# Kernel tuning notes

Hardware: AMD Instinct MI355X
Metric: run time of the kernel (lower is better)

## Reference

```python
import jax, jax.numpy as jnp
import numpy as np

D_MODEL = 1024
NUM_HEADS = 16
D_K = D_MODEL // NUM_HEADS
TEMPERATURE = 1.0
LN_EPS = 1e-5


def setup_inputs() -> dict:
    key = jax.random.key(0)
    ks = jax.random.split(key, 12)
    B, S, D = 4, 1024, D_MODEL
    w = lambda k: jax.random.normal(k, (D, D), dtype=jnp.float32) * 0.02
    b = lambda k: jax.random.normal(k, (D,), dtype=jnp.float32) * 0.01
    return {
        "query": jax.random.normal(ks[0], (B, S, D), dtype=jnp.float32),
        "key": jax.random.normal(ks[1], (B, S, D), dtype=jnp.float32),
        "value": jax.random.normal(ks[2], (B, S, D), dtype=jnp.float32),
        "wq": w(ks[3]), "bq": b(ks[4]),
        "wk": w(ks[5]), "bk": b(ks[6]),
        "wv": w(ks[7]), "bv": b(ks[8]),
        "wo": w(ks[9]), "bo": b(ks[10]),
        "temporal_bias": jax.random.normal(ks[11], (1, 1, NUM_HEADS, 1, 1), dtype=jnp.float32) * 0.01,
        "adaptive_temp": jnp.ones((1,), dtype=jnp.float32),
        "ln_gamma": jnp.ones((D,), dtype=jnp.float32),
        "ln_beta": jnp.zeros((D,), dtype=jnp.float32),
    }


def reference(query, key, value, wq, bq, wk, bk, wv, bv, wo, bo,
              temporal_bias, adaptive_temp, ln_gamma, ln_beta):
    B, S, D = query.shape
    H, dk = NUM_HEADS, D_K
    # QKV projections -> (B, H, S, dk)
    Q = (query @ wq.T + bq).reshape(B, S, H, dk).transpose(0, 2, 1, 3)
    K = (key @ wk.T + bk).reshape(B, S, H, dk).transpose(0, 2, 1, 3)
    V = (value @ wv.T + bv).reshape(B, S, H, dk).transpose(0, 2, 1, 3)
    scores = jnp.einsum('bhqd,bhkd->bhqk', Q, K) / jnp.sqrt(jnp.float32(dk))
    scores = scores / (TEMPERATURE * adaptive_temp)
    # torch broadcasting bug reproduced: (B,H,S,S) + (1,1,H,1,1) -> (1,B,H,S,S)
    scores5 = scores[None, ...] + temporal_bias  # (1, B, H, S, S)
    attn = jax.nn.softmax(scores5, axis=-1)      # (1, B, H, S, S)
    ctx5 = jnp.einsum('xbhqk,bhkd->xbhqd', attn, V)  # (1, B, H, S, dk)
    # torch: transpose(1,2) -> (1, H, B, S, dk), then view(B, S, D)
    ctx = jnp.swapaxes(ctx5, 1, 2).reshape(B, S, D)
    out = ctx @ wo.T + bo
    y = out + query
    mu = jnp.mean(y, axis=-1, keepdims=True)
    var = jnp.mean(jnp.square(y - mu), axis=-1, keepdims=True)
    out_ln = (y - mu) / jnp.sqrt(var + LN_EPS) * ln_gamma + ln_beta
    return out_ln, attn
```

## Files before the change

kernel.cpp:

```cpp
#include <hip/hip_runtime.h>
#include <math.h>

#define BB 4
#define SS 1024
#define DD 1024
#define HH 16
#define DKK 64
#define NN (BB*SS)
#define LN_EPS 1e-5f
#define QB 128
#define JB 64

typedef __attribute__((ext_vector_type(8))) short bf16x8;
typedef __attribute__((ext_vector_type(4))) float f32x4;
typedef __attribute__((address_space(3))) unsigned int lds_u32;
typedef const __attribute__((address_space(1))) unsigned int glb_u32;

static __device__ __forceinline__ unsigned short f2bf(float x){
    unsigned int u = __float_as_uint(x);
    u += 0x7fff + ((u >> 16) & 1);
    return (unsigned short)(u >> 16);
}
static __device__ __forceinline__ int swzp(int q){
    return ((q & 7) << 4) ^ ((q & 8) << 2);
}
static __device__ __forceinline__ void sync_lds_only(){
    __builtin_amdgcn_sched_barrier(0);
    asm volatile("s_waitcnt lgkmcnt(0)" ::: "memory");
    __builtin_amdgcn_s_barrier();
    __builtin_amdgcn_sched_barrier(0);
}

__global__ __launch_bounds__(256)
void k_cvt_all(const float* __restrict__ q, const float* __restrict__ k,
               const float* __restrict__ v, const float* __restrict__ w0,
               const float* __restrict__ w1, const float* __restrict__ w2,
               const float* __restrict__ w3, unsigned short* __restrict__ xout,
               unsigned short* __restrict__ wout){
    const int bidx = blockIdx.x;
    const float* src; unsigned short* dst; size_t i;
    if (bidx < 6144) {
        const int z = bidx >> 11, bi = bidx & 2047;
        src = (z == 0) ? q : (z == 1) ? k : v;
        dst = xout + (size_t)z*NN*DD;
        i = ((size_t)bi*256 + threadIdx.x)*8;
    } else {
        const int z = (bidx - 6144) >> 9, bi = (bidx - 6144) & 511;
        src = (z == 0) ? w0 : (z == 1) ? w1 : (z == 2) ? w2 : w3;
        dst = wout + (size_t)z*DD*DD;
        i = ((size_t)bi*256 + threadIdx.x)*8;
    }
    float4 a = *reinterpret_cast<const float4*>(&src[i]);
    float4 b = *reinterpret_cast<const float4*>(&src[i+4]);
    int4 w;
    w.x = (int)((unsigned)f2bf(a.x) | ((unsigned)f2bf(a.y) << 16));
    w.y = (int)((unsigned)f2bf(a.z) | ((unsigned)f2bf(a.w) << 16));
    w.z = (int)((unsigned)f2bf(b.x) | ((unsigned)f2bf(b.y) << 16));
    w.w = (int)((unsigned)f2bf(b.z) | ((unsigned)f2bf(b.w) << 16));
    *reinterpret_cast<int4*>(&dst[i]) = w;
}

__global__ __launch_bounds__(256)
void k_gemmqkv(const unsigned short* __restrict__ Xb, const unsigned short* __restrict__ Wb,
               const float* __restrict__ b0, const float* __restrict__ b1,
               const float* __restrict__ b2, unsigned short* __restrict__ outb)
{
    __shared__ __align__(16) unsigned short Als[128*32];
    __shared__ __align__(16) unsigned short Bls[128*32];
    __shared__ __align__(16) unsigned short Cs[128*128];
    const int z = blockIdx.z;
    const unsigned short* X = Xb + (size_t)z*NN*DD;
    const unsigned short* W = Wb + (size_t)z*DD*DD;
    const float* bias = (z == 0) ? b0 : (z == 1) ? b1 : b2;
    unsigned short* out = outb + (size_t)z*NN*DD;

    const int row0 = blockIdx.x * 128;
    const int col0 = blockIdx.y * 128;
    const int t = threadIdx.x;
    const int w = t >> 6, l = t & 63;
    const int wr = w >> 1, wc = w & 1;

    f32x4 acc[4][4];
    #pragma unroll
    for (int m=0;m<4;++m)
        #pragma unroll
        for (int n=0;n<4;++n) acc[m][n] = (f32x4){0.f,0.f,0.f,0.f};

    const int srow  = l >> 2;
    const int skoff = (l & 3) * 8;

    for (int kt = 0; kt < DD; kt += 32) {
        #pragma unroll
        for (int i=0;i<2;++i) {
            const unsigned short* ga = X + (size_t)(row0 + w*32 + i*16 + srow)*DD + kt + skoff;
            const unsigned short* gb = W + (size_t)(col0 + w*32 + i*16 + srow)*DD + kt + skoff;
            __builtin_amdgcn_global_load_lds((glb_u32*)ga, (lds_u32*)&Als[(w*2+i)*512], 16, 0, 0);
            __builtin_amdgcn_global_load_lds((glb_u32*)gb, (lds_u32*)&Bls[(w*2+i)*512], 16, 0, 0);
        }
        __syncthreads();
        bf16x8 af[4], bfr[4];
        #pragma unroll
        for (int m=0;m<4;++m)
            af[m] = *reinterpret_cast<const bf16x8*>(&Als[(wr*64 + m*16 + (l&15))*32 + (l>>4)*8]);
        #pragma unroll
        for (int n=0;n<4;++n)
            bfr[n] = *reinterpret_cast<const bf16x8*>(&Bls[(wc*64 + n*16 + (l&15))*32 + (l>>4)*8]);
        __builtin_amdgcn_s_setprio(1);
        #pragma unroll
        for (int m=0;m<4;++m)
            #pragma unroll
            for (int n=0;n<4;++n)
                acc[m][n] = __builtin_amdgcn_mfma_f32_16x16x32_bf16(af[m], bfr[n], acc[m][n], 0, 0, 0);
        __builtin_amdgcn_s_setprio(0);
        __syncthreads();
    }

    if (z < 2) {
        #pragma unroll
        for (int m=0;m<4;++m){
            const int trb = wr*64 + m*16 + ((l>>4)<<2);
            #pragma unroll
            for (int n=0;n<4;++n){
                const int tc = wc*64 + n*16 + (l&15);
                const float bc = bias[col0 + tc];
                #pragma unroll
                for (int r=0;r<4;++r){
                    const int tr = trb + r;
                    *reinterpret_cast<unsigned short*>(
                        (char*)Cs + ((tr*256 + tc*2) ^ ((tr & 12) << 3))) = f2bf(acc[m][n][r] + bc);
                }
            }
        }
        __syncthreads();
        #pragma unroll
        for (int i=0;i<8;++i){
            const int slot = i*256 + t;
            const int r2 = slot >> 4, g = slot & 15;
            int4 v = *reinterpret_cast<const int4*>(
                (char*)Cs + ((r2*256 + g*16) ^ ((r2 & 12) << 3)));
            *reinterpret_cast<int4*>(&out[(size_t)(row0 + r2)*DD + col0 + g*8]) = v;
        }
    } else {
        #pragma unroll
        for (int m=0;m<4;++m){
            const int trb = wr*64 + m*16 + ((l>>4)<<2);
            #pragma unroll
            for (int n=0;n<4;++n){
                const int tc = wc*64 + n*16 + (l&15);
                const float bc = bias[col0 + tc];
                ushort4 pk;
                pk.x = f2bf(acc[m][n][0] + bc);
                pk.y = f2bf(acc[m][n][1] + bc);
                pk.z = f2bf(acc[m][n][2] + bc);
                pk.w = f2bf(acc[m][n][3] + bc);
                *reinterpret_cast<ushort4*>(
                    (char*)Cs + ((tc*256 + trb*2) ^ ((tc & 15) << 3))) = pk;
            }
        }
        __syncthreads();
        const int b = row0 >> 10;
        const int sbase = row0 & 1023;
        #pragma unroll
        for (int i=0;i<16;++i){
            const int cr = i*8 + (t>>5);
            const int ch = t & 31;
            ushort4 v = *reinterpret_cast<const ushort4*>(
                (char*)Cs + ((cr*256 + ch*8) ^ ((cr & 15) << 3)));
            const int gc = col0 + cr, h = gc >> 6, k = gc & 63;
            *reinterpret_cast<ushort4*>(
                &out[(((size_t)b*HH + h)*DKK + k)*SS + sbase + ch*4]) = v;
        }
    }
}

__global__ __launch_bounds__(512)
void k_attn(const unsigned short* __restrict__ Qb, const unsigned short* __restrict__ Kb,
            const unsigned short* __restrict__ Vtb, const float* __restrict__ at,
            float* __restrict__ attn, unsigned short* __restrict__ ctxb)
{
    __shared__ __align__(16) unsigned short Qs[QB*64];
    __shared__ __align__(16) unsigned short Ks[2][JB*64];
    __shared__ __align__(16) unsigned short Vs[2][DKK*JB];
    __shared__ __align__(16) unsigned short Ps[QB*JB];
    const int f   = blockIdx.x;
    const int wk2 = (f & 7)*64 + (f >> 3);
    const int bh  = wk2 >> 3;
    const int q0  = (wk2 & 7) * QB;
    const int b = bh >> 4, h = bh & 15;
    const int t = threadIdx.x, w = t >> 6, l = t & 63;
    const float alpha = 0.125f / at[0];

    const unsigned short* Qg = Qb  + (size_t)b*SS*DD + (size_t)h*64;
    const unsigned short* Kg = Kb  + (size_t)b*SS*DD + (size_t)h*64;
    const unsigned short* Vg = Vtb + (size_t)bh*DKK*SS;

    const int sj  = t >> 3;
    const int skc = (t & 7) * 8;

    #pragma unroll
    for (int p = 0; p < 2; ++p) {
        const int c = t + p*512;
        const int q = c >> 3, kc = (c & 7) * 8;
        int4 v = *reinterpret_cast<const int4*>(&Qg[(size_t)(q0 + q)*DD + kc]);
        *reinterpret_cast<int4*>((char*)Qs + ((q*128 + kc*2) ^ ((q & 7) << 4))) = v;
    }
    {
        int4 kv = *reinterpret_cast<const int4*>(&Kg[(size_t)sj*DD + skc]);
        *reinterpret_cast<int4*>((char*)Ks[0] + ((sj*128 + skc*2) ^ ((sj & 7) << 4))) = kv;
    }
    __syncthreads();
    bf16x8 qf[2];
    {
        const int q = w*16 + (l & 15);
        #pragma unroll
        for (int ks = 0; ks < 2; ++ks)
            qf[ks] = *reinterpret_cast<const bf16x8*>(
                (char*)Qs + ((q*128 + (l>>4)*16 + ks*64) ^ ((q & 7) << 4)));
    }

    float srow = 0.f;
    int cur = 0;
    for (int j0 = 0; j0 < SS; j0 += JB) {
        int4 knext;
        const bool more = (j0 + JB < SS);
        if (more)
            knext = *reinterpret_cast<const int4*>(&Kg[(size_t)(j0 + JB + sj)*DD + skc]);
        f32x4 acc[4];
        #pragma unroll
        for (int n = 0; n < 4; ++n) acc[n] = (f32x4){0.f,0.f,0.f,0.f};
        __builtin_amdgcn_s_setprio(1);
        #pragma unroll
        for (int ks = 0; ks < 2; ++ks) {
            #pragma unroll
            for (int n = 0; n < 4; ++n) {
                const int j = n*16 + (l & 15);
                bf16x8 kf = *reinterpret_cast<const bf16x8*>(
                    (char*)Ks[cur] + ((j*128 + (l>>4)*16 + ks*64) ^ ((j & 7) << 4)));
                acc[n] = __builtin_amdgcn_mfma_f32_16x16x32_bf16(kf, qf[ks], acc[n], 0, 0, 0);
            }
        }
        __builtin_amdgcn_s_setprio(0);
        float ps = 0.f;
        #pragma unroll
        for (int n = 0; n < 4; ++n)
            #pragma unroll
            for (int r = 0; r < 4; ++r) ps += __expf(acc[n][r]*alpha);
        srow += ps;
        if (more)
            *reinterpret_cast<int4*>((char*)Ks[cur^1] + ((sj*128 + skc*2) ^ ((sj & 7) << 4))) = knext;
        __syncthreads();
        cur ^= 1;
    }
    srow += __shfl_xor(srow, 16, 64);
    srow += __shfl_xor(srow, 32, 64);
    const float sinv = 1.0f / srow;

    f32x4 cacc[4];
    #pragma unroll
    for (int n = 0; n < 4; ++n) cacc[n] = (f32x4){0.f,0.f,0.f,0.f};

    int4 knext, vnext;
    {
        int4 kv = *reinterpret_cast<const int4*>(&Kg[(size_t)sj*DD + skc]);
        int4 vv = *reinterpret_cast<const int4*>(&Vg[(size_t)sj*SS + skc]);
        *reinterpret_cast<int4*>((char*)Ks[0] + ((sj*128 + skc*2) ^ ((sj & 7) << 4))) = kv;
        *reinterpret_cast<int4*>((char*)Vs[0] + ((sj*128 + skc*2) ^ ((sj & 7) << 4))) = vv;
        knext = *reinterpret_cast<const int4*>(&Kg[(size_t)(JB + sj)*DD + skc]);
        vnext = *reinterpret_cast<const int4*>(&Vg[(size_t)sj*SS + JB + skc]);
    }
    __syncthreads();

    cur = 0;
    for (int j0 = 0; j0 < SS; j0 += JB) {
        const bool more = (j0 + JB < SS);
        f32x4 acc[4];
        #pragma unroll
        for (int n = 0; n < 4; ++n) acc[n] = (f32x4){0.f,0.f,0.f,0.f};
        __builtin_amdgcn_s_setprio(1);
        #pragma unroll
        for (int ks = 0; ks < 2; ++ks) {
            #pragma unroll
            for (int n = 0; n < 4; ++n) {
                const int j = n*16 + (l & 15);
                bf16x8 kf = *reinterpret_cast<const bf16x8*>(
                    (char*)Ks[cur] + ((j*128 + (l>>4)*16 + ks*64) ^ ((j & 7) << 4)));
                acc[n] = __builtin_amdgcn_mfma_f32_16x16x32_bf16(kf, qf[ks], acc[n], 0, 0, 0);
            }
        }
        __builtin_amdgcn_s_setprio(0);
        {
            const int q = w*16 + (l & 15);
            const int c = l >> 4;
            #pragma unroll
            for (int n = 0; n < 4; ++n) {
                float p0 = __expf(acc[n][0]*alpha) * sinv;
                float p1 = __expf(acc[n][1]*alpha) * sinv;
                float p2 = __expf(acc[n][2]*alpha) * sinv;
                float p3 = __expf(acc[n][3]*alpha) * sinv;
                int2 pk;
                pk.x = (int)((unsigned)f2bf(p0) | ((unsigned)f2bf(p1) << 16));
                pk.y = (int)((unsigned)f2bf(p2) | ((unsigned)f2bf(p3) << 16));
                *reinterpret_cast<int2*>(
                    (char*)Ps + ((q*128 + n*32 + c*8) ^ swzp(q))) = pk;
            }
        }
        if (more) {
            *reinterpret_cast<int4*>((char*)Ks[cur^1] + ((sj*128 + skc*2) ^ ((sj & 7) << 4))) = knext;
            *reinterpret_cast<int4*>((char*)Vs[cur^1] + ((sj*128 + skc*2) ^ ((sj & 7) << 4))) = vnext;
        }
        sync_lds_only();
        if (j0 + 2*JB < SS) {
            knext = *reinterpret_cast<const int4*>(&Kg[(size_t)(j0 + 2*JB + sj)*DD + skc]);
            vnext = *reinterpret_cast<const int4*>(&Vg[(size_t)sj*SS + j0 + 2*JB + skc]);
        }
        __builtin_amdgcn_s_setprio(1);
        #pragma unroll
        for (int ks = 0; ks < 2; ++ks) {
            const int qr = w*16 + (l & 15);
            bf16x8 pf = *reinterpret_cast<const bf16x8*>(
                (char*)Ps + ((qr*128 + (l>>4)*16 + ks*64) ^ swzp(qr)));
            #pragma unroll
            for (int n = 0; n < 4; ++n) {
                const int d = n*16 + (l & 15);
                bf16x8 vf = *reinterpret_cast<const bf16x8*>(
                    (char*)Vs[cur] + ((d*128 + (l>>4)*16 + ks*64) ^ ((d & 7) << 4)));
                cacc[n] = __builtin_amdgcn_mfma_f32_16x16x32_bf16(pf, vf, cacc[n], 0, 0, 0);
            }
        }
        __builtin_amdgcn_s_setprio(0);
        #pragma unroll
        for (int i = 0; i < 4; ++i) {
            const int sr = i*32 + (t >> 4);
            const int j4 = (t & 15) * 4;
            int2 u = *reinterpret_cast<const int2*>(
                (char*)Ps + ((sr*128 + j4*2) ^ swzp(sr)));
            f32x4 fv;
            fv.x = __uint_as_float(((unsigned)u.x) << 16);
            fv.y = __uint_as_float(((unsigned)u.x) & 0xffff0000u);
            fv.z = __uint_as_float(((unsigned)u.y) << 16);
            fv.w = __uint_as_float(((unsigned)u.y) & 0xffff0000u);
            __builtin_nontemporal_store(fv, reinterpret_cast<f32x4*>(
                &attn[((size_t)bh*SS + q0 + sr)*SS + j0 + j4]));
        }
        sync_lds_only();
        cur ^= 1;
    }

    #pragma unroll
    for (int n = 0; n < 4; ++n) {
        const int d = n*16 + (l & 15);
        #pragma unroll
        for (int r = 0; r < 4; ++r) {
            const int q = q0 + w*16 + (l>>4)*4 + r;
            ctxb[(((size_t)h*BB + b)*SS + q)*DKK + d] = f2bf(cacc[n][r]);
        }
    }
}

__global__ __launch_bounds__(256)
void k_gemmo(const unsigned short* __restrict__ X, const unsigned short* __restrict__ W,
             const float* __restrict__ bias, const float* __restrict__ resid,
             float* __restrict__ outf)
{
    __shared__ __align__(16) unsigned short Als[128*32];
    __shared__ __align__(16) unsigned short Bls[128*32];
    const int row0 = blockIdx.x * 128;
    const int col0 = blockIdx.y * 128;
    const int t = threadIdx.x;
    const int w = t >> 6, l = t & 63;
    const int wr = w >> 1, wc = w & 1;

    f32x4 acc[4][4];
    #pragma unroll
    for (int m=0;m<4;++m)
        #pragma unroll
        for (int n=0;n<4;++n) acc[m][n] = (f32x4){0.f,0.f,0.f,0.f};

    const int srow  = l >> 2;
    const int skoff = (l & 3) * 8;

    for (int kt = 0; kt < DD; kt += 32) {
        #pragma unroll
        for (int i=0;i<2;++i) {
            const unsigned short* ga = X + (size_t)(row0 + w*32 + i*16 + srow)*DD + kt + skoff;
            const unsigned short* gb = W + (size_t)(col0 + w*32 + i*16 + srow)*DD + kt + skoff;
            __builtin_amdgcn_global_load_lds((glb_u32*)ga, (lds_u32*)&Als[(w*2+i)*512], 16, 0, 0);
            __builtin_amdgcn_global_load_lds((glb_u32*)gb, (lds_u32*)&Bls[(w*2+i)*512], 16, 0, 0);
        }
        __syncthreads();
        bf16x8 af[4], bfr[4];
        #pragma unroll
        for (int m=0;m<4;++m)
            af[m] = *reinterpret_cast<const bf16x8*>(&Als[(wr*64 + m*16 + (l&15))*32 + (l>>4)*8]);
        #pragma unroll
        for (int n=0;n<4;++n)
            bfr[n] = *reinterpret_cast<const bf16x8*>(&Bls[(wc*64 + n*16 + (l&15))*32 + (l>>4)*8]);
        __builtin_amdgcn_s_setprio(1);
        #pragma unroll
        for (int m=0;m<4;++m)
            #pragma unroll
            for (int n=0;n<4;++n)
                acc[m][n] = __builtin_amdgcn_mfma_f32_16x16x32_bf16(af[m], bfr[n], acc[m][n], 0, 0, 0);
        __builtin_amdgcn_s_setprio(0);
        __syncthreads();
    }

    #pragma unroll
    for (int m=0;m<4;++m){
        const int grow_base = row0 + wr*64 + m*16 + ((l>>4)<<2);
        #pragma unroll
        for (int n=0;n<4;++n){
            const int col = col0 + wc*64 + n*16 + (l&15);
            const float bc = bias[col];
            #pragma unroll
            for (int r=0;r<4;++r){
                const int row = grow_base + r;
                outf[(size_t)row*DD + col] = acc[m][n][r] + bc + resid[(size_t)row*DD + col];
            }
        }
    }
}

__global__ __launch_bounds__(256)
void k_ln(const float* __restrict__ y, const float* __restrict__ g,
          const float* __restrict__ be, float* __restrict__ out)
{
    const int row = blockIdx.x;
    const int t = threadIdx.x;
    float4 v = *reinterpret_cast<const float4*>(&y[(size_t)row*DD + t*4]);
    float s  = v.x + v.y + v.z + v.w;
    float ss = v.x*v.x + v.y*v.y + v.z*v.z + v.w*v.w;
    #pragma unroll
    for (int off = 32; off > 0; off >>= 1) {
        s  += __shfl_xor(s,  off, 64);
        ss += __shfl_xor(ss, off, 64);
    }
    __shared__ float red[8];
    const int lane = t & 63, wid = t >> 6;
    if (lane == 0) { red[wid] = s; red[4+wid] = ss; }
    __syncthreads();
    const float S1 = red[0]+red[1]+red[2]+red[3];
    const float S2 = red[4]+red[5]+red[6]+red[7];
    const float mu  = S1 * (1.0f/DD);
    const float var = fmaxf(S2 * (1.0f/DD) - mu*mu, 0.0f);
    const float rstd = rsqrtf(var + LN_EPS);
    float4 gv = *reinterpret_cast<const float4*>(&g[t*4]);
    float4 bv = *reinterpret_cast<const float4*>(&be[t*4]);
    float4 o;
    o.x = (v.x - mu)*rstd*gv.x + bv.x;
    o.y = (v.y - mu)*rstd*gv.y + bv.y;
    o.z = (v.z - mu)*rstd*gv.z + bv.z;
    o.w = (v.w - mu)*rstd*gv.w + bv.w;
    *reinterpret_cast<float4*>(&out[(size_t)row*DD + t*4]) = o;
}

extern "C" void kernel_launch(void* const* d_in, const int* in_sizes, int n_in,
                              void* d_out, int out_size, void* d_ws, size_t ws_size,
                              hipStream_t stream) {
    const float* query = (const float*)d_in[0];
    const float* key   = (const float*)d_in[1];
    const float* value = (const float*)d_in[2];
    const float* wq = (const float*)d_in[3];
    const float* bq = (const float*)d_in[4];
    const float* wk = (const float*)d_in[5];
    const float* bk = (const float*)d_in[6];
    const float* wv = (const float*)d_in[7];
    const float* bv = (const float*)d_in[8];
    const float* wo = (const float*)d_in[9];
    const float* bo = (const float*)d_in[10];
    const float* at = (const float*)d_in[12];
    const float* g  = (const float*)d_in[13];
    const float* be = (const float*)d_in[14];

    float* out_ln = (float*)d_out;
    float* attn   = (float*)d_out + (size_t)NN*DD;

    char* wsb = (char*)d_ws;
    unsigned short* xq   = (unsigned short*)(wsb);
    unsigned short* Qb   = (unsigned short*)(wsb + ((size_t)24<<20));
    unsigned short* Kb   = (unsigned short*)(wsb + ((size_t)32<<20));
    unsigned short* Vtb  = (unsigned short*)(wsb + ((size_t)40<<20));
    unsigned short* ctxb = (unsigned short*)(wsb + ((size_t)48<<20));
    unsigned short* wqb  = (unsigned short*)(wsb + ((size_t)56<<20));
    float*          y    = (float*)(wsb);

    k_cvt_all<<<8192, 256, 0, stream>>>(query, key, value, wq, wk, wv, wo, xq, wqb);

    k_gemmqkv<<<dim3(32, 8, 3), 256, 0, stream>>>(xq, wqb, bq, bk, bv, Qb);

    k_attn<<<dim3(512), 512, 0, stream>>>(Qb, Kb, Vtb, at, attn, ctxb);

    k_gemmo<<<dim3(32, 8), 256, 0, stream>>>(ctxb, wqb + (size_t)3*DD*DD, bo, query, y);

    k_ln<<<NN, 256, 0, stream>>>(y, g, be, out_ln);
}
```

Baseline: 175.0 us.

## Split softmax row-sum pass into separate high-parallelism kernel

Moves the first pass of the attention kernel (QK^T plus exp row sums) into a new k_sums kernel. It launches 2048 blocks, each covering 64 queries and half the key range, and writes partial sums to workspace. k_attn then loads Q fragments straight from global memory and reads the two partial sums, so only the second pass remains. The aim is more parallelism and occupancy for the reduction pass. In exchange it adds a kernel launch and a small workspace round trip, and recomputes QK^T just as the old first pass did.

```diff
diff --git a/kernel.cpp b/kernel.cpp
--- a/kernel.cpp
+++ b/kernel.cpp
@@ -173,12 +173,90 @@
     }
 }
 
+__global__ __launch_bounds__(256)
+void k_sums(const unsigned short* __restrict__ Qb, const unsigned short* __restrict__ Kb,
+            const float* __restrict__ at, float* __restrict__ rsums)
+{
+    __shared__ __align__(16) unsigned short Ks[2][JB*64];
+    const int f   = blockIdx.x;
+    const int swz = (f & 7)*256 + (f >> 3);
+    const int bh  = swz >> 5;
+    const int qt  = (swz >> 1) & 15;
+    const int jh  = swz & 1;
+    const int b = bh >> 4, h = bh & 15;
+    const int t = threadIdx.x, w = t >> 6, l = t & 63;
+    const float alpha = 0.125f / at[0];
+
+    const unsigned short* Qg = Qb + (size_t)b*SS*DD + (size_t)h*64;
+    const unsigned short* Kg = Kb + (size_t)b*SS*DD + (size_t)h*64;
+    const int q0 = qt*64;
+    const int jbase = jh*512;
+
+    const int sj  = t >> 2;
+    const int skc = (t & 3) * 16;
+
+    bf16x8 qf[2];
+    const int qrow = q0 + w*16 + (l & 15);
+    #pragma unroll
+    for (int ks = 0; ks < 2; ++ks)
+        qf[ks] = *reinterpret_cast<const bf16x8*>(
+            &Qg[(size_t)qrow*DD + ks*32 + (l>>4)*8]);
+
+    {
+        int4 kv0 = *reinterpret_cast<const int4*>(&Kg[(size_t)(jbase + sj)*DD + skc]);
+        int4 kv1 = *reinterpret_cast<const int4*>(&Kg[(size_t)(jbase + sj)*DD + skc + 8]);
+        *reinterpret_cast<int4*>((char*)Ks[0] + ((sj*128 + skc*2)      ^ ((sj & 7) << 4))) = kv0;
+        *reinterpret_cast<int4*>((char*)Ks[0] + ((sj*128 + skc*2 + 16) ^ ((sj & 7) << 4))) = kv1;
+    }
+    __syncthreads();
+
+    float srow = 0.f;
+    int cur = 0;
+    for (int jt = 0; jt < 512; jt += JB) {
+        int4 k0, k1;
+        const bool more = (jt + JB < 512);
+        if (more) {
+            k0 = *reinterpret_cast<const int4*>(&Kg[(size_t)(jbase + jt + JB + sj)*DD + skc]);
+            k1 = *reinterpret_cast<const int4*>(&Kg[(size_t)(jbase + jt + JB + sj)*DD + skc + 8]);
+        }
+        f32x4 acc[4];
+        #pragma unroll
+        for (int n = 0; n < 4; ++n) acc[n] = (f32x4){0.f,0.f,0.f,0.f};
+        __builtin_amdgcn_s_setprio(1);
+        #pragma unroll
+        for (int ks = 0; ks < 2; ++ks) {
+            #pragma unroll
+            for (int n = 0; n < 4; ++n) {
+                const int j = n*16 + (l & 15);
+                bf16x8 kf = *reinterpret_cast<const bf16x8*>(
+                    (char*)Ks[cur] + ((j*128 + (l>>4)*16 + ks*64) ^ ((j & 7) << 4)));
+                acc[n] = __builtin_amdgcn_mfma_f32_16x16x32_bf16(kf, qf[ks], acc[n], 0, 0, 0);
+            }
+        }
+        __builtin_amdgcn_s_setprio(0);
+        #pragma unroll
+        for (int n = 0; n < 4; ++n)
+            #pragma unroll
+            for (int r = 0; r < 4; ++r) srow += __expf(acc[n][r]*alpha);
+        if (more) {
+            *reinterpret_cast<int4*>((char*)Ks[cur^1] + ((sj*128 + skc*2)      ^ ((sj & 7) << 4))) = k0;
+            *reinterpret_cast<int4*>((char*)Ks[cur^1] + ((sj*128 + skc*2 + 16) ^ ((sj & 7) << 4))) = k1;
+        }
+        __syncthreads();
+        cur ^= 1;
+    }
+    srow += __shfl_xor(srow, 16, 64);
+    srow += __shfl_xor(srow, 32, 64);
+    if ((l >> 4) == 0)
+        rsums[((size_t)bh*2 + jh)*SS + qrow] = srow;
+}
+
 __global__ __launch_bounds__(512)
 void k_attn(const unsigned short* __restrict__ Qb, const unsigned short* __restrict__ Kb,
             const unsigned short* __restrict__ Vtb, const float* __restrict__ at,
+            const float* __restrict__ rsums,
             float* __restrict__ attn, unsigned short* __restrict__ ctxb)
 {
-    __shared__ __align__(16) unsigned short Qs[QB*64];
     __shared__ __align__(16) unsigned short Ks[2][JB*64];
     __shared__ __align__(16) unsigned short Vs[2][DKK*JB];
     __shared__ __align__(16) unsigned short Ps[QB*JB];
@@ -197,63 +275,14 @@
     const int sj  = t >> 3;
     const int skc = (t & 7) * 8;
 
-    #pragma unroll
-    for (int p = 0; p < 2; ++p) {
-        const int c = t + p*512;
-        const int q = c >> 3, kc = (c & 7) * 8;
-        int4 v = *reinterpret_cast<const int4*>(&Qg[(size_t)(q0 + q)*DD + kc]);
-        *reinterpret_cast<int4*>((char*)Qs + ((q*128 + kc*2) ^ ((q & 7) << 4))) = v;
-    }
-    {
-        int4 kv = *reinterpret_cast<const int4*>(&Kg[(size_t)sj*DD + skc]);
-        *reinterpret_cast<int4*>((char*)Ks[0] + ((sj*128 + skc*2) ^ ((sj & 7) << 4))) = kv;
-    }
-    __syncthreads();
     bf16x8 qf[2];
-    {
-        const int q = w*16 + (l & 15);
-        #pragma unroll
-        for (int ks = 0; ks < 2; ++ks)
-            qf[ks] = *reinterpret_cast<const bf16x8*>(
-                (char*)Qs + ((q*128 + (l>>4)*16 + ks*64) ^ ((q & 7) << 4)));
-    }
-
-    float srow = 0.f;
-    int cur = 0;
-    for (int j0 = 0; j0 < SS; j0 += JB) {
-        int4 knext;
-        const bool more = (j0 + JB < SS);
-        if (more)
-            knext = *reinterpret_cast<const int4*>(&Kg[(size_t)(j0 + JB + sj)*DD + skc]);
-        f32x4 acc[4];
-        #pragma unroll
-        for (int n = 0; n < 4; ++n) acc[n] = (f32x4){0.f,0.f,0.f,0.f};
-        __builtin_amdgcn_s_setprio(1);
-        #pragma unroll
-        for (int ks = 0; ks < 2; ++ks) {
-            #pragma unroll
-            for (int n = 0; n < 4; ++n) {
-                const int j = n*16 + (l & 15);
-                bf16x8 kf = *reinterpret_cast<const bf16x8*>(
-                    (char*)Ks[cur] + ((j*128 + (l>>4)*16 + ks*64) ^ ((j & 7) << 4)));
-                acc[n] = __builtin_amdgcn_mfma_f32_16x16x32_bf16(kf, qf[ks], acc[n], 0, 0, 0);
-            }
-        }
-        __builtin_amdgcn_s_setprio(0);
-        float ps = 0.f;
-        #pragma unroll
-        for (int n = 0; n < 4; ++n)
-            #pragma unroll
-            for (int r = 0; r < 4; ++r) ps += __expf(acc[n][r]*alpha);
-        srow += ps;
-        if (more)
-            *reinterpret_cast<int4*>((char*)Ks[cur^1] + ((sj*128 + skc*2) ^ ((sj & 7) << 4))) = knext;
-        __syncthreads();
-        cur ^= 1;
-    }
-    srow += __shfl_xor(srow, 16, 64);
-    srow += __shfl_xor(srow, 32, 64);
-    const float sinv = 1.0f / srow;
+    const int qrow = q0 + w*16 + (l & 15);
+    #pragma unroll
+    for (int ks = 0; ks < 2; ++ks)
+        qf[ks] = *reinterpret_cast<const bf16x8*>(
+            &Qg[(size_t)qrow*DD + ks*32 + (l>>4)*8]);
+    const float sinv = 1.0f /
+        (rsums[((size_t)bh*2 + 0)*SS + qrow] + rsums[((size_t)bh*2 + 1)*SS + qrow]);
 
     f32x4 cacc[4];
     #pragma unroll
@@ -270,7 +299,7 @@
     }
     __syncthreads();
 
-    cur = 0;
+    int cur = 0;
     for (int j0 = 0; j0 < SS; j0 += JB) {
         const bool more = (j0 + JB < SS);
         f32x4 acc[4];
@@ -483,12 +512,15 @@
     unsigned short* ctxb = (unsigned short*)(wsb + ((size_t)48<<20));
     unsigned short* wqb  = (unsigned short*)(wsb + ((size_t)56<<20));
     float*          y    = (float*)(wsb);
+    float*          rsums= (float*)(wsb + ((size_t)20<<20));
 
     k_cvt_all<<<8192, 256, 0, stream>>>(query, key, value, wq, wk, wv, wo, xq, wqb);
 
     k_gemmqkv<<<dim3(32, 8, 3), 256, 0, stream>>>(xq, wqb, bq, bk, bv, Qb);
 
-    k_attn<<<dim3(512), 512, 0, stream>>>(Qb, Kb, Vtb, at, attn, ctxb);
+    k_sums<<<dim3(2048), 256, 0, stream>>>(Qb, Kb, at, rsums);
+
+    k_attn<<<dim3(512), 512, 0, stream>>>(Qb, Kb, Vtb, at, rsums, attn, ctxb);
 
     k_gemmo<<<dim3(32, 8), 256, 0, stream>>>(ctxb, wqb + (size_t)3*DD*DD, bo, query, y);
 
```

Measured after the change: 189.2 us. 8.1% more time.

## Halve attention query tile to 64 rows with 256-thread blocks and direct Q loads

Applied to the files above, without the earlier changes.

Shrinks the attention block from 128 query rows and 512 threads to 64 rows and 256 threads, doubling the grid to 1024 blocks. Q fragments are now read straight from global memory into registers, so the Q shared-memory tile is gone. Each thread loads two 16-byte K/V chunks per stage instead of one. The aim is more resident blocks per CU and less LDS use, at the cost of reloading K and V twice as often across blocks.

```diff
diff --git a/kernel.cpp b/kernel.cpp
--- a/kernel.cpp
+++ b/kernel.cpp
@@ -8,7 +8,7 @@
 #define DKK 64
 #define NN (BB*SS)
 #define LN_EPS 1e-5f
-#define QB 128
+#define QB 64
 #define JB 64
 
 typedef __attribute__((ext_vector_type(8))) short bf16x8;
@@ -173,19 +173,18 @@
     }
 }
 
-__global__ __launch_bounds__(512)
+__global__ __launch_bounds__(256)
 void k_attn(const unsigned short* __restrict__ Qb, const unsigned short* __restrict__ Kb,
             const unsigned short* __restrict__ Vtb, const float* __restrict__ at,
             float* __restrict__ attn, unsigned short* __restrict__ ctxb)
 {
-    __shared__ __align__(16) unsigned short Qs[QB*64];
     __shared__ __align__(16) unsigned short Ks[2][JB*64];
     __shared__ __align__(16) unsigned short Vs[2][DKK*JB];
     __shared__ __align__(16) unsigned short Ps[QB*JB];
     const int f   = blockIdx.x;
-    const int wk2 = (f & 7)*64 + (f >> 3);
-    const int bh  = wk2 >> 3;
-    const int q0  = (wk2 & 7) * QB;
+    const int wk2 = (f & 7)*128 + (f >> 3);
+    const int bh  = wk2 >> 4;
+    const int q0  = (wk2 & 15) * QB;
     const int b = bh >> 4, h = bh & 15;
     const int t = threadIdx.x, w = t >> 6, l = t & 63;
     const float alpha = 0.125f / at[0];
@@ -194,37 +193,33 @@
     const unsigned short* Kg = Kb  + (size_t)b*SS*DD + (size_t)h*64;
     const unsigned short* Vg = Vtb + (size_t)bh*DKK*SS;
 
-    const int sj  = t >> 3;
-    const int skc = (t & 7) * 8;
-
-    #pragma unroll
-    for (int p = 0; p < 2; ++p) {
-        const int c = t + p*512;
-        const int q = c >> 3, kc = (c & 7) * 8;
-        int4 v = *reinterpret_cast<const int4*>(&Qg[(size_t)(q0 + q)*DD + kc]);
-        *reinterpret_cast<int4*>((char*)Qs + ((q*128 + kc*2) ^ ((q & 7) << 4))) = v;
-    }
+    const int sj  = t >> 2;
+    const int skc = (t & 3) * 16;
+
+    bf16x8 qf[2];
+    const int qrow = q0 + w*16 + (l & 15);
+    #pragma unroll
+    for (int ks = 0; ks < 2; ++ks)
+        qf[ks] = *reinterpret_cast<const bf16x8*>(
+            &Qg[(size_t)qrow*DD + ks*32 + (l>>4)*8]);
+
     {
-        int4 kv = *reinterpret_cast<const int4*>(&Kg[(size_t)sj*DD + skc]);
-        *reinterpret_cast<int4*>((char*)Ks[0] + ((sj*128 + skc*2) ^ ((sj & 7) << 4))) = kv;
+        int4 k0 = *reinterpret_cast<const int4*>(&Kg[(size_t)sj*DD + skc]);
+        int4 k1 = *reinterpret_cast<const int4*>(&Kg[(size_t)sj*DD + skc + 8]);
+        *reinterpret_cast<int4*>((char*)Ks[0] + ((sj*128 + skc*2)      ^ ((sj & 7) << 4))) = k0;
+        *reinterpret_cast<int4*>((char*)Ks[0] + ((sj*128 + skc*2 + 16) ^ ((sj & 7) << 4))) = k1;
     }
     __syncthreads();
-    bf16x8 qf[2];
-    {
-        const int q = w*16 + (l & 15);
-        #pragma unroll
-        for (int ks = 0; ks < 2; ++ks)
-            qf[ks] = *reinterpret_cast<const bf16x8*>(
-                (char*)Qs + ((q*128 + (l>>4)*16 + ks*64) ^ ((q & 7) << 4)));
-    }
 
     float srow = 0.f;
     int cur = 0;
     for (int j0 = 0; j0 < SS; j0 += JB) {
-        int4 knext;
+        int4 kn0, kn1;
         const bool more = (j0 + JB < SS);
-        if (more)
-            knext = *reinterpret_cast<const int4*>(&Kg[(size_t)(j0 + JB + sj)*DD + skc]);
+        if (more) {
+            kn0 = *reinterpret_cast<const int4*>(&Kg[(size_t)(j0 + JB + sj)*DD + skc]);
+            kn1 = *reinterpret_cast<const int4*>(&Kg[(size_t)(j0 + JB + sj)*DD + skc + 8]);
+        }
         f32x4 acc[4];
         #pragma unroll
         for (int n = 0; n < 4; ++n) acc[n] = (f32x4){0.f,0.f,0.f,0.f};
@@ -240,14 +235,14 @@
             }
         }
         __builtin_amdgcn_s_setprio(0);
-        float ps = 0.f;
         #pragma unroll
         for (int n = 0; n < 4; ++n)
             #pragma unroll
-            for (int r = 0; r < 4; ++r) ps += __expf(acc[n][r]*alpha);
-        srow += ps;
-        if (more)
-            *reinterpret_cast<int4*>((char*)Ks[cur^1] + ((sj*128 + skc*2) ^ ((sj & 7) << 4))) = knext;
+            for (int r = 0; r < 4; ++r) srow += __expf(acc[n][r]*alpha);
+        if (more) {
+            *reinterpret_cast<int4*>((char*)Ks[cur^1] + ((sj*128 + skc*2)      ^ ((sj & 7) << 4))) = kn0;
+            *reinterpret_cast<int4*>((char*)Ks[cur^1] + ((sj*128 + skc*2 + 16) ^ ((sj & 7) << 4))) = kn1;
+        }
         __syncthreads();
         cur ^= 1;
     }
@@ -259,14 +254,20 @@
     #pragma unroll
     for (int n = 0; n < 4; ++n) cacc[n] = (f32x4){0.f,0.f,0.f,0.f};
 
-    int4 knext, vnext;
+    int4 kn0, kn1, vn0, vn1;
     {
-        int4 kv = *reinterpret_cast<const int4*>(&Kg[(size_t)sj*DD + skc]);
-        int4 vv = *reinterpret_cast<const int4*>(&Vg[(size_t)sj*SS + skc]);
-        *reinterpret_cast<int4*>((char*)Ks[0] + ((sj*128 + skc*2) ^ ((sj & 7) << 4))) = kv;
-        *reinterpret_cast<int4*>((char*)Vs[0] + ((sj*128 + skc*2) ^ ((sj & 7) << 4))) = vv;
-        knext = *reinterpret_cast<const int4*>(&Kg[(size_t)(JB + sj)*DD + skc]);
-        vnext = *reinterpret_cast<const int4*>(&Vg[(size_t)sj*SS + JB + skc]);
+        int4 k0 = *reinterpret_cast<const int4*>(&Kg[(size_t)sj*DD + skc]);
+        int4 k1 = *reinterpret_cast<const int4*>(&Kg[(size_t)sj*DD + skc + 8]);
+        int4 v0 = *reinterpret_cast<const int4*>(&Vg[(size_t)sj*SS + skc]);
+        int4 v1 = *reinterpret_cast<const int4*>(&Vg[(size_t)sj*SS + skc + 8]);
+        *reinterpret_cast<int4*>((char*)Ks[0] + ((sj*128 + skc*2)      ^ ((sj & 7) << 4))) = k0;
+        *reinterpret_cast<int4*>((char*)Ks[0] + ((sj*128 + skc*2 + 16) ^ ((sj & 7) << 4))) = k1;
+        *reinterpret_cast<int4*>((char*)Vs[0] + ((sj*128 + skc*2)      ^ ((sj & 7) << 4))) = v0;
+        *reinterpret_cast<int4*>((char*)Vs[0] + ((sj*128 + skc*2 + 16) ^ ((sj & 7) << 4))) = v1;
+        kn0 = *reinterpret_cast<const int4*>(&Kg[(size_t)(JB + sj)*DD + skc]);
+        kn1 = *reinterpret_cast<const int4*>(&Kg[(size_t)(JB + sj)*DD + skc + 8]);
+        vn0 = *reinterpret_cast<const int4*>(&Vg[(size_t)sj*SS + JB + skc]);
+        vn1 = *reinterpret_cast<const int4*>(&Vg[(size_t)sj*SS + JB + skc + 8]);
     }
     __syncthreads();
 
@@ -305,13 +306,17 @@
             }
         }
         if (more) {
-            *reinterpret_cast<int4*>((char*)Ks[cur^1] + ((sj*128 + skc*2) ^ ((sj & 7) << 4))) = knext;
-            *reinterpret_cast<int4*>((char*)Vs[cur^1] + ((sj*128 + skc*2) ^ ((sj & 7) << 4))) = vnext;
+            *reinterpret_cast<int4*>((char*)Ks[cur^1] + ((sj*128 + skc*2)      ^ ((sj & 7) << 4))) = kn0;
+            *reinterpret_cast<int4*>((char*)Ks[cur^1] + ((sj*128 + skc*2 + 16) ^ ((sj & 7) << 4))) = kn1;
+            *reinterpret_cast<int4*>((char*)Vs[cur^1] + ((sj*128 + skc*2)      ^ ((sj & 7) << 4))) = vn0;
+            *reinterpret_cast<int4*>((char*)Vs[cur^1] + ((sj*128 + skc*2 + 16) ^ ((sj & 7) << 4))) = vn1;
         }
         sync_lds_only();
         if (j0 + 2*JB < SS) {
-            knext = *reinterpret_cast<const int4*>(&Kg[(size_t)(j0 + 2*JB + sj)*DD + skc]);
-            vnext = *reinterpret_cast<const int4*>(&Vg[(size_t)sj*SS + j0 + 2*JB + skc]);
+            kn0 = *reinterpret_cast<const int4*>(&Kg[(size_t)(j0 + 2*JB + sj)*DD + skc]);
+            kn1 = *reinterpret_cast<const int4*>(&Kg[(size_t)(j0 + 2*JB + sj)*DD + skc + 8]);
+            vn0 = *reinterpret_cast<const int4*>(&Vg[(size_t)sj*SS + j0 + 2*JB + skc]);
+            vn1 = *reinterpret_cast<const int4*>(&Vg[(size_t)sj*SS + j0 + 2*JB + skc + 8]);
         }
         __builtin_amdgcn_s_setprio(1);
         #pragma unroll
@@ -330,7 +335,7 @@
         __builtin_amdgcn_s_setprio(0);
         #pragma unroll
         for (int i = 0; i < 4; ++i) {
-            const int sr = i*32 + (t >> 4);
+            const int sr = i*16 + (t >> 4);
             const int j4 = (t & 15) * 4;
             int2 u = *reinterpret_cast<const int2*>(
                 (char*)Ps + ((sr*128 + j4*2) ^ swzp(sr)));
@@ -488,7 +493,7 @@
 
     k_gemmqkv<<<dim3(32, 8, 3), 256, 0, stream>>>(xq, wqb, bq, bk, bv, Qb);
 
-    k_attn<<<dim3(512), 512, 0, stream>>>(Qb, Kb, Vtb, at, attn, ctxb);
+    k_attn<<<dim3(1024), 256, 0, stream>>>(Qb, Kb, Vtb, at, attn, ctxb);
 
     k_gemmo<<<dim3(32, 8), 256, 0, stream>>>(ctxb, wqb + (size_t)3*DD*DD, bo, query, y);
 
```

New measurement: 177.6 us. No clear change (+1.5%).
